# Kernel tuning notes

Measured on AMD Instinct MI355X. Metric: run time of the kernel, lower is better.

Reference implementation:

```python
import jax, jax.numpy as jnp
import numpy as np

B, S, H = 8, 512, 1024
NH = 8
DH = H // NH            # 128
INTER = 3072            # DebertaConfig default intermediate_size
SPAN = 512              # max_relative_positions (= max_position_embeddings)
LSTM_H = H // 2         # 512
EPS = 1e-7              # DeBERTa layer_norm_eps


def _ln(x, g, b):
    m = jnp.mean(x, -1, keepdims=True)
    v = jnp.var(x, -1, keepdims=True)
    return (x - m) / jnp.sqrt(v + EPS) * g + b


def _lstm_dir(x, Wih, Whh, bih, bhh, reverse):
    # x: [B,S,D]; precompute input projection for all steps
    xW = jnp.einsum('bsd,gd->sbg', x, Wih) + bih + bhh      # [S,B,4*Hd]
    Hd = Whh.shape[1]

    def step(carry, gx):
        h, c = carry
        gates = gx + h @ Whh.T
        i, f, g, o = jnp.split(gates, 4, axis=-1)           # torch gate order i,f,g,o
        i = jax.nn.sigmoid(i); f = jax.nn.sigmoid(f); o = jax.nn.sigmoid(o)
        g = jnp.tanh(g)
        c = f * c + i * g
        h = o * jnp.tanh(c)
        return (h, c), h

    h0 = jnp.zeros((x.shape[0], Hd), x.dtype)
    _, hs = jax.lax.scan(step, (h0, h0), xW, reverse=reverse)
    return jnp.swapaxes(hs, 0, 1)                            # [B,S,Hd]


def setup_inputs() -> dict:
    key = jax.random.key(0)
    ks = iter(jax.random.split(key, 40))

    def rn(shape, s=0.02):
        return jax.random.normal(next(ks), shape, jnp.float32) * s

    return {
        'x': jax.random.normal(next(ks), (B, S, H), jnp.float32),
        'pos_emb': rn((SPAN, H)),
        'emb_ln_g': jnp.ones((H,), jnp.float32),
        'emb_ln_b': jnp.zeros((H,), jnp.float32),
        'in_proj_w': rn((3 * H, H)),
        'q_bias': jnp.zeros((H,), jnp.float32),
        'v_bias': jnp.zeros((H,), jnp.float32),
        'rel_emb': rn((2 * SPAN, H)),
        'pos_proj_w': rn((H, H)),
        'pos_q_proj_w': rn((H, H)),
        'pos_q_proj_b': jnp.zeros((H,), jnp.float32),
        'attn_out_w': rn((H, H)),
        'attn_out_b': jnp.zeros((H,), jnp.float32),
        'attn_ln_g': jnp.ones((H,), jnp.float32),
        'attn_ln_b': jnp.zeros((H,), jnp.float32),
        'inter_w': rn((INTER, H)),
        'inter_b': jnp.zeros((INTER,), jnp.float32),
        'ffn_out_w': rn((H, INTER)),
        'ffn_out_b': jnp.zeros((H,), jnp.float32),
        'ffn_ln_g': jnp.ones((H,), jnp.float32),
        'ffn_ln_b': jnp.zeros((H,), jnp.float32),
        'Wih_f': rn((4 * LSTM_H, H)),
        'Whh_f': rn((4 * LSTM_H, LSTM_H)),
        'bih_f': jnp.zeros((4 * LSTM_H,), jnp.float32),
        'bhh_f': jnp.zeros((4 * LSTM_H,), jnp.float32),
        'Wih_r': rn((4 * LSTM_H, H)),
        'Whh_r': rn((4 * LSTM_H, LSTM_H)),
        'bih_r': jnp.zeros((4 * LSTM_H,), jnp.float32),
        'bhh_r': jnp.zeros((4 * LSTM_H,), jnp.float32),
    }


def reference(x, pos_emb, emb_ln_g, emb_ln_b, in_proj_w, q_bias, v_bias, rel_emb,
              pos_proj_w, pos_q_proj_w, pos_q_proj_b, attn_out_w, attn_out_b,
              attn_ln_g, attn_ln_b, inter_w, inter_b, ffn_out_w, ffn_out_b,
              ffn_ln_g, ffn_ln_b, Wih_f, Whh_f, bih_f, bhh_f, Wih_r, Whh_r,
              bih_r, bhh_r):
    # ---- DeBERTa embeddings: inputs_embeds + absolute positions, LayerNorm ----
    h = _ln(x + pos_emb[None, :S], emb_ln_g, emb_ln_b)

    # ---- disentangled self-attention (c2p + p2c) ----
    qkv = h @ in_proj_w.T                                    # [B,S,3H]
    q, k, v = jnp.split(qkv, 3, -1)
    q = q + q_bias
    v = v + v_bias

    def heads(t):
        return t.reshape(B, S, NH, DH).transpose(0, 2, 1, 3)  # [B,NH,S,DH]
    q, k, v = heads(q), heads(k), heads(v)

    scale_factor = 3.0                                       # 1 + len(['c2p','p2c'])
    q = q / jnp.sqrt(jnp.float32(DH) * scale_factor)
    scores = jnp.einsum('bhqd,bhkd->bhqk', q, k)             # [B,NH,S,S]

    rel_pos = jnp.arange(S)[:, None] - jnp.arange(S)[None, :]  # [S,S]

    # content -> position
    c2p_idx = jnp.clip(rel_pos + SPAN, 0, 2 * SPAN - 1)
    pos_key = (rel_emb @ pos_proj_w.T).reshape(2 * SPAN, NH, DH)
    c2p = jnp.einsum('bhqd,rhd->bhqr', q, pos_key)           # [B,NH,S,2*SPAN]
    c2p = jnp.take_along_axis(c2p, jnp.broadcast_to(c2p_idx[None, None], (B, NH, S, S)), axis=-1)

    # position -> content
    pos_q = (rel_emb @ pos_q_proj_w.T + pos_q_proj_b).reshape(2 * SPAN, NH, DH)
    pos_q = pos_q / jnp.sqrt(jnp.float32(DH) * scale_factor)
    p2c_idx = jnp.clip(-rel_pos + SPAN, 0, 2 * SPAN - 1)
    p2c = jnp.einsum('bhkd,rhd->bhkr', k, pos_q)             # [B,NH,S,2*SPAN]
    p2c = jnp.take_along_axis(p2c, jnp.broadcast_to(p2c_idx[None, None], (B, NH, S, S)), axis=-1)
    p2c = jnp.swapaxes(p2c, -1, -2)

    probs = jax.nn.softmax(scores + c2p + p2c, -1)
    ctx = jnp.einsum('bhqk,bhkd->bhqd', probs, v).transpose(0, 2, 1, 3).reshape(B, S, H)

    h = _ln(ctx @ attn_out_w.T + attn_out_b + h, attn_ln_g, attn_ln_b)
    inter = jax.nn.gelu(h @ inter_w.T + inter_b, approximate=False)
    h = _ln(inter @ ffn_out_w.T + ffn_out_b + h, ffn_ln_g, ffn_ln_b)

    # ---- bidirectional single-layer LSTM ----
    hf = _lstm_dir(h, Wih_f, Whh_f, bih_f, bhh_f, False)
    hr = _lstm_dir(h, Wih_r, Whh_r, bih_r, bhh_r, True)
    return jnp.concatenate([hf, hr], -1)                     # [B,S,H]
```

## Files before the change

kernel.cpp:

```cpp
#include <hip/hip_runtime.h>
#include <cstdint>


typedef __bf16 bf8_t __attribute__((ext_vector_type(8)));
typedef float f32x4 __attribute__((ext_vector_type(4)));
typedef unsigned int u32x4 __attribute__((ext_vector_type(4)));

__device__ __forceinline__ unsigned short f2bf(float f) {
  union { float f; unsigned int u; } v; v.f = f;
  unsigned int r = v.u + 0x7fffu + ((v.u >> 16) & 1u);
  return (unsigned short)(r >> 16);
}
__device__ __forceinline__ float bf2f(unsigned short s) {
  union { unsigned int u; float f; } v; v.u = ((unsigned int)s) << 16;
  return v.f;
}
__device__ __forceinline__ float bflo(unsigned int u) {
  union { unsigned int u; float f; } v; v.u = u << 16; return v.f;
}
__device__ __forceinline__ float bfhi(unsigned int u) {
  union { unsigned int u; float f; } v; v.u = u & 0xffff0000u; return v.f;
}

__device__ __forceinline__ void async16(const void* g, void* l) {
  __builtin_amdgcn_global_load_lds(
      (const __attribute__((address_space(1))) void*)g,
      (__attribute__((address_space(3))) void*)l, 16, 0, 0);
}

__device__ __forceinline__ void ld2_ic(const unsigned short* p0,
                                       const unsigned short* p1,
                                       u32x4& r0, u32x4& r1) {
  asm volatile("global_load_dwordx4 %0, %2, off sc0 sc1\n\t"
               "global_load_dwordx4 %1, %3, off sc0 sc1\n\t"
               "s_waitcnt vmcnt(0)"
               : "=v"(r0), "=v"(r1)
               : "v"(p0), "v"(p1)
               : "memory");
}
__device__ __forceinline__ void st_ic(unsigned short* p, u32x4 v) {
  asm volatile("global_store_dwordx4 %0, %1, off sc0 sc1"
               :: "v"(p), "v"(v) : "memory");
}

__global__ void k_sentinel(float* out) { out[0] = 1e30f; }

__global__ void k_cast_bf16(const float* __restrict__ in, unsigned short* __restrict__ out) {
  long i = ((long)blockIdx.x * 256 + threadIdx.x) * 4;
  float4 v = *(const float4*)(in + i);
  unsigned int a = (unsigned int)f2bf(v.x) | ((unsigned int)f2bf(v.y) << 16);
  unsigned int b = (unsigned int)f2bf(v.z) | ((unsigned int)f2bf(v.w) << 16);
  *(uint2*)(out + i) = make_uint2(a, b);
}

__global__ void k_build_bias(const float* qb, const float* vb, float* qkvBias,
                             const float* bihf, const float* bhhf, float* bsf,
                             const float* bihr, const float* bhhr, float* bsr) {
  int i = blockIdx.x * 256 + threadIdx.x;
  if (i < 3072) {
    float v;
    if (i < 1024) v = qb[i];
    else if (i < 2048) v = 0.f;
    else v = vb[i - 2048];
    qkvBias[i] = v;
  }
  if (i < 2048) {
    bsf[i] = bihf[i] + bhhf[i];
    bsr[i] = bihr[i] + bhhr[i];
  }
}

__global__ __launch_bounds__(256) void k_layernorm(
    const float* __restrict__ in, const float* __restrict__ res, unsigned int resMask,
    const float* __restrict__ gamma, const float* __restrict__ beta,
    float* __restrict__ outF, unsigned short* __restrict__ outB) {
  const int row = blockIdx.x;
  const int tid = threadIdx.x;
  float4 v = ((const float4*)(in + (long)row * 1024))[tid];
  if (res) {
    float4 r = ((const float4*)(res + (long)(row & resMask) * 1024))[tid];
    v.x += r.x; v.y += r.y; v.z += r.z; v.w += r.w;
  }
  float s = v.x + v.y + v.z + v.w;
  float q = v.x * v.x + v.y * v.y + v.z * v.z + v.w * v.w;
#pragma unroll
  for (int o = 32; o; o >>= 1) { s += __shfl_down(s, o); q += __shfl_down(q, o); }
  __shared__ float rs[4], rq[4];
  const int wave = tid >> 6, lane = tid & 63;
  if (lane == 0) { rs[wave] = s; rq[wave] = q; }
  __syncthreads();
  s = rs[0] + rs[1] + rs[2] + rs[3];
  q = rq[0] + rq[1] + rq[2] + rq[3];
  const float mean = s * (1.f / 1024.f);
  const float var = q * (1.f / 1024.f) - mean * mean;
  const float rstd = rsqrtf(var + 1e-7f);
  float4 g4 = ((const float4*)gamma)[tid];
  float4 b4 = ((const float4*)beta)[tid];
  float4 o4;
  o4.x = (v.x - mean) * rstd * g4.x + b4.x;
  o4.y = (v.y - mean) * rstd * g4.y + b4.y;
  o4.z = (v.z - mean) * rstd * g4.z + b4.z;
  o4.w = (v.w - mean) * rstd * g4.w + b4.w;
  if (outF) ((float4*)(outF + (long)row * 1024))[tid] = o4;
  if (outB) {
    unsigned int a = (unsigned int)f2bf(o4.x) | ((unsigned int)f2bf(o4.y) << 16);
    unsigned int b = (unsigned int)f2bf(o4.z) | ((unsigned int)f2bf(o4.w) << 16);
    ((uint2*)(outB + (long)row * 1024))[tid] = make_uint2(a, b);
  }
}

template <int MODE>
__global__ __launch_bounds__(256) void k_gemm_bt(
    const unsigned short* __restrict__ A, int lda,
    const unsigned short* __restrict__ Bm, int ldb,
    void* __restrict__ Cv, int ldc,
    int K, const float* __restrict__ bias, float scale) {
  __shared__ __align__(16) unsigned short As[128 * 32];
  __shared__ __align__(16) unsigned short Bs[128 * 32];
  const int tid = threadIdx.x;
  const int lane = tid & 63;
  const int wave = tid >> 6;
  const int n0 = blockIdx.x * 128;
  const int m0 = blockIdx.y * 128;
  const int srow = tid >> 2;
  const int scol = (tid & 3) * 8;
  const unsigned short* ag0 = A + (long)(m0 + srow) * lda + scol;
  const unsigned short* ag1 = A + (long)(m0 + 64 + srow) * lda + scol;
  const unsigned short* bg0 = Bm + (long)(n0 + srow) * ldb + scol;
  const unsigned short* bg1 = Bm + (long)(n0 + 64 + srow) * ldb + scol;
  unsigned short* asd0 = &As[(wave * 16) * 32];
  unsigned short* asd1 = &As[(64 + wave * 16) * 32];
  unsigned short* bsd0 = &Bs[(wave * 16) * 32];
  unsigned short* bsd1 = &Bs[(64 + wave * 16) * 32];
  const int wm = wave >> 1, wn = wave & 1;
  const int mrow = lane & 15;
  const int kq = (lane >> 4) * 8;
  const f32x4 vzero = {0.f, 0.f, 0.f, 0.f};
  f32x4 acc[4][4];
#pragma unroll
  for (int i = 0; i < 4; ++i)
#pragma unroll
    for (int j = 0; j < 4; ++j) acc[i][j] = vzero;

  const int nk = K >> 5;
  for (int kt = 0; kt < nk; ++kt) {
    if (kt) __syncthreads();
    async16(ag0, asd0); async16(ag1, asd1);
    async16(bg0, bsd0); async16(bg1, bsd1);
    ag0 += 32; ag1 += 32; bg0 += 32; bg1 += 32;
    __syncthreads();
    bf8_t af[4], bf[4];
#pragma unroll
    for (int i = 0; i < 4; ++i)
      af[i] = *(const bf8_t*)&As[(wm * 64 + i * 16 + mrow) * 32 + kq];
#pragma unroll
    for (int j = 0; j < 4; ++j)
      bf[j] = *(const bf8_t*)&Bs[(wn * 64 + j * 16 + mrow) * 32 + kq];
#pragma unroll
    for (int i = 0; i < 4; ++i)
#pragma unroll
      for (int j = 0; j < 4; ++j)
        acc[i][j] = __builtin_amdgcn_mfma_f32_16x16x32_bf16(af[i], bf[j], acc[i][j], 0, 0, 0);
  }
  const int quad = lane >> 4;
  const int cn = lane & 15;
  float* Cf = (float*)Cv;
  unsigned short* Cb = (unsigned short*)Cv;
#pragma unroll
  for (int i = 0; i < 4; ++i) {
#pragma unroll
    for (int j = 0; j < 4; ++j) {
#pragma unroll
      for (int r = 0; r < 4; ++r) {
        int row = m0 + wm * 64 + i * 16 + quad * 4 + r;
        int col = n0 + wn * 64 + j * 16 + cn;
        float v = acc[i][j][r];
        if (bias) v += bias[col];
        v *= scale;
        if (MODE == 2) v = 0.5f * v * (1.0f + erff(v * 0.70710678118654752f));
        long idx = (long)row * ldc + col;
        if (MODE == 0) Cf[idx] = v;
        else Cb[idx] = f2bf(v);
      }
    }
  }
}

__global__ __launch_bounds__(256) void k_attention(
    const unsigned short* __restrict__ qkv,
    const unsigned short* __restrict__ c2p,
    const unsigned short* __restrict__ p2c,
    unsigned short* __restrict__ ctx, int h) {
  const int tid = threadIdx.x;
  const int qt = blockIdx.x;
  const int b = blockIdx.y;
  const int q0 = qt * 16;
  __shared__ __align__(16) float sc[16][520];
  __shared__ __align__(16) float qs[16][128];

  for (int i = tid; i < 16 * 128; i += 256) {
    int ql = i >> 7, d = i & 127;
    qs[ql][d] = bf2f(qkv[((long)(b * 512 + q0 + ql)) * 3072 + h * 128 + d]);
  }
  __syncthreads();

  const float scale = 0.051031036307982884f;
  for (int pass = 0; pass < 2; ++pass) {
    const int k = tid + pass * 256;
    float4 kvf[32];
    const unsigned short* kp = qkv + ((long)(b * 512 + k)) * 3072 + 1024 + h * 128;
#pragma unroll
    for (int c = 0; c < 16; ++c) {
      uint4 u = ((const uint4*)kp)[c];
      kvf[2 * c + 0] = make_float4(bflo(u.x), bfhi(u.x), bflo(u.y), bfhi(u.y));
      kvf[2 * c + 1] = make_float4(bflo(u.z), bfhi(u.z), bflo(u.w), bfhi(u.w));
    }
    const unsigned short* pp = p2c + ((long)(b * 512 + k)) * 1024 + (q0 - k + 512);
    for (int ql = 0; ql < 16; ++ql) {
      float dot = 0.f;
#pragma unroll
      for (int dd = 0; dd < 32; ++dd) {
        float4 qf = ((const float4*)&qs[ql][0])[dd];
        dot += qf.x * kvf[dd].x + qf.y * kvf[dd].y + qf.z * kvf[dd].z + qf.w * kvf[dd].w;
      }
      sc[ql][k] = dot * scale + bf2f(pp[ql]);
    }
  }
  __syncthreads();

  const int wave = tid >> 6, lane = tid & 63;
#pragma unroll
  for (int rr = 0; rr < 4; ++rr) {
    const int r = wave * 4 + rr;
    const int q = q0 + r;
    const unsigned short* cp = c2p + ((long)(b * 512 + q)) * 1024 + (q + 512);
    float v[8];
#pragma unroll
    for (int i = 0; i < 8; ++i) {
      int k = lane + 64 * i;
      v[i] = sc[r][k] + bf2f(cp[-k]);
    }
    float m = v[0];
#pragma unroll
    for (int i = 1; i < 8; ++i) m = fmaxf(m, v[i]);
#pragma unroll
    for (int o = 32; o; o >>= 1) m = fmaxf(m, __shfl_xor(m, o));
    float ssum = 0.f;
#pragma unroll
    for (int i = 0; i < 8; ++i) { v[i] = __expf(v[i] - m); ssum += v[i]; }
#pragma unroll
    for (int o = 32; o; o >>= 1) ssum += __shfl_xor(ssum, o);
    const float inv = 1.0f / ssum;
#pragma unroll
    for (int i = 0; i < 8; ++i) sc[r][lane + 64 * i] = v[i] * inv;
  }
  __syncthreads();

  const int d = tid & 127;
  const int qg = tid >> 7;
  float acc[8] = {0, 0, 0, 0, 0, 0, 0, 0};
  const unsigned short* vp = qkv + ((long)(b * 512)) * 3072 + 2048 + h * 128 + d;
  for (int k = 0; k < 512; k += 4) {
    float v0 = bf2f(vp[(long)(k + 0) * 3072]);
    float v1 = bf2f(vp[(long)(k + 1) * 3072]);
    float v2 = bf2f(vp[(long)(k + 2) * 3072]);
    float v3 = bf2f(vp[(long)(k + 3) * 3072]);
#pragma unroll
    for (int qq = 0; qq < 8; ++qq) {
      float4 p = *(const float4*)&sc[qg * 8 + qq][k];
      acc[qq] += p.x * v0 + p.y * v1 + p.z * v2 + p.w * v3;
    }
  }
#pragma unroll
  for (int qq = 0; qq < 8; ++qq) {
    int q = q0 + qg * 8 + qq;
    ctx[((long)(b * 512 + q)) * 1024 + h * 128 + d] = f2bf(acc[qq]);
  }
}

__global__ __launch_bounds__(256) void k_lstm(
    const float* __restrict__ WhhF, const float* __restrict__ WhhR,
    const unsigned short* __restrict__ xWF, const unsigned short* __restrict__ xWR,
    float* __restrict__ out, unsigned short* __restrict__ hx) {
  const int tid = threadIdx.x;
  const int lane = tid & 63;
  const int g = tid >> 6;
  const int dir = blockIdx.y;
  const int j0 = blockIdx.x * 16;
  const float* Whh = dir ? WhhR : WhhF;
  const unsigned short* xW = dir ? xWR : xWF;
  unsigned short* hxd = hx + (long)dir * 512 * 4096;

  __shared__ __align__(16) unsigned short hT[16][520];
  __shared__ float gl[4][16][8];
  __shared__ __align__(16) unsigned short hs[8][16];

  const int m = lane & 15, quad = lane >> 4;
  bf8_t afr[16];
  {
    const float* wr = Whh + ((long)(g * 512 + j0 + m)) * 512 + quad * 8;
#pragma unroll
    for (int kt = 0; kt < 16; ++kt) {
      float4 f0 = *(const float4*)(wr + kt * 32);
      float4 f1 = *(const float4*)(wr + kt * 32 + 4);
      bf8_t a;
      a[0] = (__bf16)f0.x; a[1] = (__bf16)f0.y; a[2] = (__bf16)f0.z; a[3] = (__bf16)f0.w;
      a[4] = (__bf16)f1.x; a[5] = (__bf16)f1.y; a[6] = (__bf16)f1.z; a[7] = (__bf16)f1.w;
      afr[kt] = a;
    }
  }
  for (int i = tid; i < 16 * 520; i += 256) (&hT[0][0])[i] = 0;
  float cstate = 0.f;
  __syncthreads();

  for (int se = 0; se < 512; ++se) {
    const int s = dir ? 511 - se : se;
    uint2 uxw = make_uint2(0u, 0u);
    if (m < 8)
      uxw = *(const uint2*)(xW + ((long)(m * 512 + s)) * 2048 + g * 512 + j0 + quad * 4);

    if (se) {
      const int sp = dir ? s + 1 : s - 1;
      const unsigned short* hxs = hxd + (long)sp * 4096;
      const unsigned short* p0 = hxs + (2 * g) * 512 + lane * 8;
      const unsigned short* p1 = hxs + (2 * g + 1) * 512 + lane * 8;
      u32x4 r0, r1;
      for (;;) {
        ld2_ic(p0, p1, r0, r1);
        bool ok = true;
#pragma unroll
        for (int t = 0; t < 4; ++t) {
          ok = ok && (r0[t] & 0xffffu) && (r0[t] >> 16) &&
               (r1[t] & 0xffffu) && (r1[t] >> 16);
        }
        if (__ballot(ok) == 0xFFFFFFFFFFFFFFFFull) break;
      }
      *(u32x4*)&hT[2 * g][lane * 8] = r0;
      *(u32x4*)&hT[2 * g + 1][lane * 8] = r1;
      __syncthreads();
    }

    f32x4 a0 = {0.f, 0.f, 0.f, 0.f}, a1 = a0, a2 = a0, a3 = a0;
#pragma unroll
    for (int t = 0; t < 4; ++t) {
      bf8_t b0 = *(const bf8_t*)&hT[m][(4 * t + 0) * 32 + quad * 8];
      bf8_t b1 = *(const bf8_t*)&hT[m][(4 * t + 1) * 32 + quad * 8];
      bf8_t b2 = *(const bf8_t*)&hT[m][(4 * t + 2) * 32 + quad * 8];
      bf8_t b3 = *(const bf8_t*)&hT[m][(4 * t + 3) * 32 + quad * 8];
      a0 = __builtin_amdgcn_mfma_f32_16x16x32_bf16(afr[4 * t + 0], b0, a0, 0, 0, 0);
      a1 = __builtin_amdgcn_mfma_f32_16x16x32_bf16(afr[4 * t + 1], b1, a1, 0, 0, 0);
      a2 = __builtin_amdgcn_mfma_f32_16x16x32_bf16(afr[4 * t + 2], b2, a2, 0, 0, 0);
      a3 = __builtin_amdgcn_mfma_f32_16x16x32_bf16(afr[4 * t + 3], b3, a3, 0, 0, 0);
    }
    if (m < 8) {
      gl[g][quad * 4 + 0][m] = a0[0] + a1[0] + a2[0] + a3[0] + bflo(uxw.x);
      gl[g][quad * 4 + 1][m] = a0[1] + a1[1] + a2[1] + a3[1] + bfhi(uxw.x);
      gl[g][quad * 4 + 2][m] = a0[2] + a1[2] + a2[2] + a3[2] + bflo(uxw.y);
      gl[g][quad * 4 + 3][m] = a0[3] + a1[3] + a2[3] + a3[3] + bfhi(uxw.y);
    }
    __syncthreads();
    if (tid < 128) {
      const int jj = tid >> 3, bb = tid & 7;
      float iv = gl[0][jj][bb], fv = gl[1][jj][bb];
      float gv = gl[2][jj][bb], ov = gl[3][jj][bb];
      float is = 1.f / (1.f + __expf(-iv));
      float fs = 1.f / (1.f + __expf(-fv));
      float gt = 2.f / (1.f + __expf(-2.f * gv)) - 1.f;
      float os = 1.f / (1.f + __expf(-ov));
      cstate = fs * cstate + is * gt;
      float hv = os * (2.f / (1.f + __expf(-2.f * cstate)) - 1.f);
      hs[bb][jj] = f2bf(hv) | 1;
      out[((long)(bb * 512 + s)) * 1024 + dir * 512 + j0 + jj] = hv;
    }
    __syncthreads();
    if (tid < 16) {
      const int b = tid >> 1, half = tid & 1;
      st_ic(hxd + (long)s * 4096 + b * 512 + j0 + half * 8,
            *(const u32x4*)&hs[b][half * 8]);
    }
  }
}

extern "C" void kernel_launch(void* const* d_in, const int* in_sizes, int n_in,
                              void* d_out, int out_size, void* d_ws, size_t ws_size,
                              hipStream_t stream) {
  const float* x         = (const float*)d_in[0];
  const float* pos_emb   = (const float*)d_in[1];
  const float* emb_ln_g  = (const float*)d_in[2];
  const float* emb_ln_b  = (const float*)d_in[3];
  const float* in_proj_w = (const float*)d_in[4];
  const float* q_bias    = (const float*)d_in[5];
  const float* v_bias    = (const float*)d_in[6];
  const float* rel_emb   = (const float*)d_in[7];
  const float* pos_proj_w   = (const float*)d_in[8];
  const float* pos_q_proj_w = (const float*)d_in[9];
  const float* pos_q_proj_b = (const float*)d_in[10];
  const float* attn_out_w = (const float*)d_in[11];
  const float* attn_out_b = (const float*)d_in[12];
  const float* attn_ln_g  = (const float*)d_in[13];
  const float* attn_ln_b  = (const float*)d_in[14];
  const float* inter_w    = (const float*)d_in[15];
  const float* inter_b    = (const float*)d_in[16];
  const float* ffn_out_w  = (const float*)d_in[17];
  const float* ffn_out_b  = (const float*)d_in[18];
  const float* ffn_ln_g   = (const float*)d_in[19];
  const float* ffn_ln_b   = (const float*)d_in[20];
  const float* Wih_f = (const float*)d_in[21];
  const float* Whh_f = (const float*)d_in[22];
  const float* bih_f = (const float*)d_in[23];
  const float* bhh_f = (const float*)d_in[24];
  const float* Wih_r = (const float*)d_in[25];
  const float* Whh_r = (const float*)d_in[26];
  const float* bih_r = (const float*)d_in[27];
  const float* bhh_r = (const float*)d_in[28];
  float* out = (float*)d_out;

  const size_t MB = 1ull << 20;
  const size_t NEED = 85 * MB;
  if (ws_size < NEED) {
    k_sentinel<<<dim3(1), dim3(1), 0, stream>>>(out);
    return;
  }
  char* ws = (char*)d_ws;
  typedef unsigned short u16;
  u16*   qkv_b    = (u16*)(ws + 0);
  float* attn_tmp = (float*)(ws + 0);
  u16*   xW_f     = (u16*)(ws + 0);
  u16*   h1_b     = (u16*)(ws + 16 * MB);
  u16*   xW_r     = (u16*)(ws + 16 * MB);
  float* h0_f     = (float*)(ws + 24 * MB);
  u16*   inter_bf = (u16*)(ws + 24 * MB);
  u16*   hx       = (u16*)(ws + 32 * MB);
  u16*   c2p_h    = (u16*)(ws + 40 * MB);
  u16*   p2c_h    = (u16*)(ws + 48 * MB);
  float* h1_f     = (float*)(ws + 48 * MB);
  u16*   h0_b     = (u16*)(ws + 64 * MB);
  u16*   ctx_b    = (u16*)(ws + 64 * MB);
  u16*   h2_b     = (u16*)(ws + 64 * MB);
  u16*   wscr     = (u16*)(ws + 72 * MB);
  u16*   relemb_b = (u16*)(ws + 78 * MB);
  u16*   poskey_b = (u16*)(ws + 80 * MB);
  u16*   posq_b   = (u16*)(ws + 82 * MB);
  float* bias_qkv = (float*)(ws + 84 * MB);
  float* bsum_f   = (float*)(ws + 84 * MB + 16 * 1024);
  float* bsum_r   = (float*)(ws + 84 * MB + 32 * 1024);
  float* ffn_tmp  = out;

  const float SCALE = 0.051031036307982884f;

  auto cast = [&](const float* src, u16* dst, long n) {
    k_cast_bf16<<<dim3((unsigned)(n / 1024)), dim3(256), 0, stream>>>(src, dst);
  };

  k_build_bias<<<dim3(12), dim3(256), 0, stream>>>(q_bias, v_bias, bias_qkv,
                                                   bih_f, bhh_f, bsum_f,
                                                   bih_r, bhh_r, bsum_r);

  k_layernorm<<<dim3(4096), dim3(256), 0, stream>>>(x, pos_emb, 511u, emb_ln_g,
                                                    emb_ln_b, h0_f, h0_b);

  cast(in_proj_w, wscr, 3145728L);
  k_gemm_bt<1><<<dim3(24, 32), dim3(256), 0, stream>>>(
      h0_b, 1024, wscr, 1024, qkv_b, 3072, 1024, bias_qkv, 1.0f);

  cast(rel_emb, relemb_b, 1048576L);
  cast(pos_proj_w, wscr, 1048576L);
  k_gemm_bt<1><<<dim3(8, 8), dim3(256), 0, stream>>>(
      relemb_b, 1024, wscr, 1024, poskey_b, 1024, 1024, (const float*)nullptr, 1.0f);
  cast(pos_q_proj_w, wscr, 1048576L);
  k_gemm_bt<1><<<dim3(8, 8), dim3(256), 0, stream>>>(
      relemb_b, 1024, wscr, 1024, posq_b, 1024, 1024, pos_q_proj_b, SCALE);

  for (int h = 0; h < 8; ++h) {
    k_gemm_bt<1><<<dim3(8, 32), dim3(256), 0, stream>>>(
        qkv_b + h * 128, 3072, poskey_b + h * 128, 1024, c2p_h, 1024, 128,
        (const float*)nullptr, SCALE);
    k_gemm_bt<1><<<dim3(8, 32), dim3(256), 0, stream>>>(
        qkv_b + 1024 + h * 128, 3072, posq_b + h * 128, 1024, p2c_h, 1024, 128,
        (const float*)nullptr, 1.0f);
    k_attention<<<dim3(32, 8), dim3(256), 0, stream>>>(qkv_b, c2p_h, p2c_h, ctx_b, h);
  }

  cast(attn_out_w, wscr, 1048576L);
  k_gemm_bt<0><<<dim3(8, 32), dim3(256), 0, stream>>>(
      ctx_b, 1024, wscr, 1024, attn_tmp, 1024, 1024, attn_out_b, 1.0f);
  k_layernorm<<<dim3(4096), dim3(256), 0, stream>>>(attn_tmp, h0_f, 0xFFFFFFFFu,
                                                    attn_ln_g, attn_ln_b, h1_f, h1_b);

  cast(inter_w, wscr, 3145728L);
  k_gemm_bt<2><<<dim3(24, 32), dim3(256), 0, stream>>>(
      h1_b, 1024, wscr, 1024, inter_bf, 3072, 1024, inter_b, 1.0f);
  cast(ffn_out_w, wscr, 3145728L);
  k_gemm_bt<0><<<dim3(8, 32), dim3(256), 0, stream>>>(
      inter_bf, 3072, wscr, 3072, ffn_tmp, 1024, 3072, ffn_out_b, 1.0f);
  hipMemsetAsync(hx, 0, 8 * MB, stream);
  k_layernorm<<<dim3(4096), dim3(256), 0, stream>>>(ffn_tmp, h1_f, 0xFFFFFFFFu,
                                                    ffn_ln_g, ffn_ln_b,
                                                    (float*)nullptr, h2_b);

  cast(Wih_f, wscr, 2097152L);
  k_gemm_bt<1><<<dim3(16, 32), dim3(256), 0, stream>>>(
      h2_b, 1024, wscr, 1024, xW_f, 2048, 1024, bsum_f, 1.0f);
  cast(Wih_r, wscr, 2097152L);
  k_gemm_bt<1><<<dim3(16, 32), dim3(256), 0, stream>>>(
      h2_b, 1024, wscr, 1024, xW_r, 2048, 1024, bsum_r, 1.0f);

  k_lstm<<<dim3(32, 2), dim3(256), 0, stream>>>(Whh_f, Whh_r, xW_f, xW_r, out, hx);

  (void)in_sizes; (void)n_in; (void)out_size;
}
```

Before: 2.312 ms.

## Poll an L2-coherent mirror buffer for LSTM hidden-state exchange across blocks

The LSTM step exchange now writes each hidden value twice, to the system-coherent buffer and to a mirror buffer with L2-scope stores. Consumers poll the mirror with L2-scope loads first and fall back to the system-coherent buffer with sleeps. The grid is reshaped to 256 blocks with dir = blockIdx & 7, and 6 of every 8 blocks exit at once. The intent appears to be placing the 64 working blocks on one XCD so they share an L2, which makes the cheaper L2-coherent loads valid. Per-thread short stores replace the shared-memory staging and one barrier. The risks are relying on an unguaranteed block-to-XCD mapping and doubling store traffic.

```diff
diff --git a/kernel.cpp b/kernel.cpp
--- a/kernel.cpp
+++ b/kernel.cpp
@@ -38,9 +38,21 @@
                : "v"(p0), "v"(p1)
                : "memory");
 }
-__device__ __forceinline__ void st_ic(unsigned short* p, u32x4 v) {
-  asm volatile("global_store_dwordx4 %0, %1, off sc0 sc1"
-               :: "v"(p), "v"(v) : "memory");
+__device__ __forceinline__ void ld2_l2(const unsigned short* p0,
+                                       const unsigned short* p1,
+                                       u32x4& r0, u32x4& r1) {
+  asm volatile("global_load_dwordx4 %0, %2, off sc0\n\t"
+               "global_load_dwordx4 %1, %3, off sc0\n\t"
+               "s_waitcnt vmcnt(0)"
+               : "=v"(r0), "=v"(r1)
+               : "v"(p0), "v"(p1)
+               : "memory");
+}
+__device__ __forceinline__ void sts_ic(unsigned short* p, unsigned int v) {
+  asm volatile("global_store_short %0, %1, off sc0 sc1" :: "v"(p), "v"(v) : "memory");
+}
+__device__ __forceinline__ void sts_l2(unsigned short* p, unsigned int v) {
+  asm volatile("global_store_short %0, %1, off sc0" :: "v"(p), "v"(v) : "memory");
 }
 
 __global__ void k_sentinel(float* out) { out[0] = 1e30f; }
@@ -281,19 +293,22 @@
 __global__ __launch_bounds__(256) void k_lstm(
     const float* __restrict__ WhhF, const float* __restrict__ WhhR,
     const unsigned short* __restrict__ xWF, const unsigned short* __restrict__ xWR,
-    float* __restrict__ out, unsigned short* __restrict__ hx) {
+    float* __restrict__ out, unsigned short* __restrict__ hx,
+    unsigned short* __restrict__ mir) {
+  const int bi = blockIdx.x;
+  const int dir = bi & 7;
+  if (dir >= 2) return;
+  const int j0 = (bi >> 3) * 16;
   const int tid = threadIdx.x;
   const int lane = tid & 63;
   const int g = tid >> 6;
-  const int dir = blockIdx.y;
-  const int j0 = blockIdx.x * 16;
   const float* Whh = dir ? WhhR : WhhF;
   const unsigned short* xW = dir ? xWR : xWF;
   unsigned short* hxd = hx + (long)dir * 512 * 4096;
+  unsigned short* mird = mir + (long)dir * 512 * 4096;
 
   __shared__ __align__(16) unsigned short hT[16][520];
-  __shared__ float gl[4][16][8];
-  __shared__ __align__(16) unsigned short hs[8][16];
+  __shared__ float gl[4][8][16];
 
   const int m = lane & 15, quad = lane >> 4;
   bf8_t afr[16];
@@ -321,12 +336,15 @@
 
     if (se) {
       const int sp = dir ? s + 1 : s - 1;
-      const unsigned short* hxs = hxd + (long)sp * 4096;
-      const unsigned short* p0 = hxs + (2 * g) * 512 + lane * 8;
-      const unsigned short* p1 = hxs + (2 * g + 1) * 512 + lane * 8;
+      const long so = (long)sp * 4096;
+      const int o0 = (2 * g) * 512 + lane * 8;
+      const int o1 = (2 * g + 1) * 512 + lane * 8;
       u32x4 r0, r1;
+      int tries = 0;
       for (;;) {
-        ld2_ic(p0, p1, r0, r1);
+        const bool useMir = (tries < 2) || (tries & 1);
+        if (useMir) ld2_l2(mird + so + o0, mird + so + o1, r0, r1);
+        else        ld2_ic(hxd + so + o0, hxd + so + o1, r0, r1);
         bool ok = true;
 #pragma unroll
         for (int t = 0; t < 4; ++t) {
@@ -334,11 +352,13 @@
                (r1[t] & 0xffffu) && (r1[t] >> 16);
         }
         if (__ballot(ok) == 0xFFFFFFFFFFFFFFFFull) break;
+        ++tries;
+        if (!useMir) __builtin_amdgcn_s_sleep(1);
       }
       *(u32x4*)&hT[2 * g][lane * 8] = r0;
       *(u32x4*)&hT[2 * g + 1][lane * 8] = r1;
-      __syncthreads();
-    }
+    }
+    __syncthreads();
 
     f32x4 a0 = {0.f, 0.f, 0.f, 0.f}, a1 = a0, a2 = a0, a3 = a0;
 #pragma unroll
@@ -353,30 +373,27 @@
       a3 = __builtin_amdgcn_mfma_f32_16x16x32_bf16(afr[4 * t + 3], b3, a3, 0, 0, 0);
     }
     if (m < 8) {
-      gl[g][quad * 4 + 0][m] = a0[0] + a1[0] + a2[0] + a3[0] + bflo(uxw.x);
-      gl[g][quad * 4 + 1][m] = a0[1] + a1[1] + a2[1] + a3[1] + bfhi(uxw.x);
-      gl[g][quad * 4 + 2][m] = a0[2] + a1[2] + a2[2] + a3[2] + bflo(uxw.y);
-      gl[g][quad * 4 + 3][m] = a0[3] + a1[3] + a2[3] + a3[3] + bfhi(uxw.y);
+      gl[g][m][quad * 4 + 0] = a0[0] + a1[0] + a2[0] + a3[0] + bflo(uxw.x);
+      gl[g][m][quad * 4 + 1] = a0[1] + a1[1] + a2[1] + a3[1] + bfhi(uxw.x);
+      gl[g][m][quad * 4 + 2] = a0[2] + a1[2] + a2[2] + a3[2] + bflo(uxw.y);
+      gl[g][m][quad * 4 + 3] = a0[3] + a1[3] + a2[3] + a3[3] + bfhi(uxw.y);
     }
     __syncthreads();
     if (tid < 128) {
-      const int jj = tid >> 3, bb = tid & 7;
-      float iv = gl[0][jj][bb], fv = gl[1][jj][bb];
-      float gv = gl[2][jj][bb], ov = gl[3][jj][bb];
+      const int bb = tid >> 4, jj = tid & 15;
+      float iv = gl[0][bb][jj], fv = gl[1][bb][jj];
+      float gv = gl[2][bb][jj], ov = gl[3][bb][jj];
       float is = 1.f / (1.f + __expf(-iv));
       float fs = 1.f / (1.f + __expf(-fv));
       float gt = 2.f / (1.f + __expf(-2.f * gv)) - 1.f;
       float os = 1.f / (1.f + __expf(-ov));
       cstate = fs * cstate + is * gt;
       float hv = os * (2.f / (1.f + __expf(-2.f * cstate)) - 1.f);
-      hs[bb][jj] = f2bf(hv) | 1;
+      unsigned int hb = (unsigned int)(f2bf(hv) | 1);
+      const long ho = (long)s * 4096 + bb * 512 + j0 + jj;
+      sts_l2(mird + ho, hb);
+      sts_ic(hxd + ho, hb);
       out[((long)(bb * 512 + s)) * 1024 + dir * 512 + j0 + jj] = hv;
-    }
-    __syncthreads();
-    if (tid < 16) {
-      const int b = tid >> 1, half = tid & 1;
-      st_ic(hxd + (long)s * 4096 + b * 512 + j0 + half * 8,
-            *(const u32x4*)&hs[b][half * 8]);
     }
   }
 }
@@ -432,6 +449,7 @@
   u16*   inter_bf = (u16*)(ws + 24 * MB);
   u16*   hx       = (u16*)(ws + 32 * MB);
   u16*   c2p_h    = (u16*)(ws + 40 * MB);
+  u16*   mir      = (u16*)(ws + 40 * MB);
   u16*   p2c_h    = (u16*)(ws + 48 * MB);
   float* h1_f     = (float*)(ws + 48 * MB);
   u16*   h0_b     = (u16*)(ws + 64 * MB);
@@ -494,6 +512,7 @@
   k_gemm_bt<0><<<dim3(8, 32), dim3(256), 0, stream>>>(
       inter_bf, 3072, wscr, 3072, ffn_tmp, 1024, 3072, ffn_out_b, 1.0f);
   hipMemsetAsync(hx, 0, 8 * MB, stream);
+  hipMemsetAsync(mir, 0, 8 * MB, stream);
   k_layernorm<<<dim3(4096), dim3(256), 0, stream>>>(ffn_tmp, h1_f, 0xFFFFFFFFu,
                                                     ffn_ln_g, ffn_ln_b,
                                                     (float*)nullptr, h2_b);
@@ -505,7 +524,7 @@
   k_gemm_bt<1><<<dim3(16, 32), dim3(256), 0, stream>>>(
       h2_b, 1024, wscr, 1024, xW_r, 2048, 1024, bsum_r, 1.0f);
 
-  k_lstm<<<dim3(32, 2), dim3(256), 0, stream>>>(Whh_f, Whh_r, xW_f, xW_r, out, hx);
+  k_lstm<<<dim3(256), dim3(256), 0, stream>>>(Whh_f, Whh_r, xW_f, xW_r, out, hx, mir);
 
   (void)in_sizes; (void)n_in; (void)out_size;
 }
```

New measurement: 2.143 ms. -7.3%, faster.
